# Performance work log

Measured on AMD Instinct MI355X. Metric: run time of the kernel, lower is better.

The kernel has to match this reference:

```python
import math
import jax, jax.numpy as jnp
import numpy as np

N = 100000
E_RAND = 800000
IN_F, HID, OUT_F, HEADS = 128, 64, 64, 4
NOISE_SCALE = 1.0 * math.sqrt(2.0 * math.log(1.25 / 0.05))  # dp_rate=1, eps=1, del=0.05


def setup_inputs() -> dict:
    key = jax.random.key(0)
    ks = jax.random.split(key, 12)
    x = jax.random.normal(ks[0], (N, IN_F), dtype=jnp.float32)
    src_r = jax.random.randint(ks[1], (E_RAND,), 0, N, dtype=jnp.int32)
    dst_r = jax.random.randint(ks[2], (E_RAND,), 0, N, dtype=jnp.int32)
    loops = jnp.arange(N, dtype=jnp.int32)  # add_self_loop
    src = jnp.concatenate([src_r, loops])
    dst = jnp.concatenate([dst_r, loops])
    # layer 0: GATConv(in=128, out=64, heads=4)
    s0 = 1.0 / math.sqrt(IN_F)
    W0 = jax.random.normal(ks[3], (IN_F, HEADS * HID), dtype=jnp.float32) * s0
    al0 = jax.random.normal(ks[4], (HEADS, HID), dtype=jnp.float32) * 0.1
    ar0 = jax.random.normal(ks[5], (HEADS, HID), dtype=jnp.float32) * 0.1
    b0 = jnp.zeros((HEADS * HID,), dtype=jnp.float32)
    # layer 1: GATConv(in=256, out=64, heads=1)
    s1 = 1.0 / math.sqrt(HEADS * HID)
    W1 = jax.random.normal(ks[6], (HEADS * HID, OUT_F), dtype=jnp.float32) * s1
    al1 = jax.random.normal(ks[7], (1, OUT_F), dtype=jnp.float32) * 0.1
    ar1 = jax.random.normal(ks[8], (1, OUT_F), dtype=jnp.float32) * 0.1
    b1 = jnp.zeros((OUT_F,), dtype=jnp.float32)
    # DP gaussian noise added after first GAT layer (torch.normal(0,1,x.shape))
    noise = jax.random.normal(ks[9], (N, HEADS * HID), dtype=jnp.float32)
    return {"x": x, "src": src, "dst": dst, "W0": W0, "al0": al0, "ar0": ar0,
            "b0": b0, "W1": W1, "al1": al1, "ar1": ar1, "b1": b1, "noise": noise}


def gat_conv(x, src, dst, W, al, ar, b, apply_act):
    """DGL GATConv: per-edge attention, edge softmax over dst, scatter-sum."""
    H, D = al.shape
    h = (x @ W).reshape(-1, H, D)                      # [N,H,D]
    el = jnp.sum(h * al, axis=-1)                      # [N,H]
    er = jnp.sum(h * ar, axis=-1)                      # [N,H]
    e = jax.nn.leaky_relu(el[src] + er[dst], 0.2)      # [E,H]
    emax = jax.ops.segment_max(e, dst, num_segments=N) # [N,H]
    a = jnp.exp(e - emax[dst])
    denom = jax.ops.segment_sum(a, dst, num_segments=N)
    alpha = a / denom[dst]                             # [E,H] edge softmax
    msg = h[src] * alpha[:, :, None]                   # [E,H,D]
    out = jax.ops.segment_sum(msg, dst, num_segments=N) + b.reshape(1, H, D)
    if apply_act:
        out = jax.nn.leaky_relu(out, 0.01)             # F.leaky_relu default slope
    return out.reshape(-1, H * D)                      # flatten(1)


def reference(x, src, dst, W0, al0, ar0, b0, W1, al1, ar1, b1, noise):
    h = gat_conv(x, src, dst, W0, al0, ar0, b0, apply_act=True)   # [N, 256]
    h = h + NOISE_SCALE * noise                                   # DP noise after layer 0
    out = gat_conv(h, src, dst, W1, al1, ar1, b1, apply_act=False)  # [N, 64]
    return out
```

## Files before the change

kernel.cpp:

```cpp
#include <hip/hip_runtime.h>
#include <hip/hip_bf16.h>
#include <math.h>

#define IN_F 128
#define HID 64
#define HEADS 4
#define HD0 (HEADS * HID)
#define OUT_F 64
#define NOISE_SCALE 2.5372725354060904f

typedef __bf16 bf16x8 __attribute__((ext_vector_type(8)));
typedef float f32x4 __attribute__((ext_vector_type(4)));

__device__ __forceinline__ float bf2f(unsigned short u) {
    return __uint_as_float(((unsigned)u) << 16);
}
__device__ __forceinline__ unsigned short f2bf(float f) {
    unsigned u = __float_as_uint(f);
    u = u + 0x7fffu + ((u >> 16) & 1u);
    return (unsigned short)(u >> 16);
}

__device__ __forceinline__ void acc8(float* acc, const uint4& u, float wt) {
    acc[0] += wt * __uint_as_float(u.x << 16);
    acc[1] += wt * __uint_as_float(u.x & 0xffff0000u);
    acc[2] += wt * __uint_as_float(u.y << 16);
    acc[3] += wt * __uint_as_float(u.y & 0xffff0000u);
    acc[4] += wt * __uint_as_float(u.z << 16);
    acc[5] += wt * __uint_as_float(u.z & 0xffff0000u);
    acc[6] += wt * __uint_as_float(u.w << 16);
    acc[7] += wt * __uint_as_float(u.w & 0xffff0000u);
}

__global__ __launch_bounds__(256) void cast_bf16_kernel(
    const float* __restrict__ in, unsigned short* __restrict__ out, size_t n8,
    int* __restrict__ deg, int N) {
    size_t i = (size_t)blockIdx.x * 256 + threadIdx.x;
    if (i < (size_t)N) deg[i] = 0;
    if (i >= n8) return;
    const float4 a = ((const float4*)in)[i * 2];
    const float4 b = ((const float4*)in)[i * 2 + 1];
    ushort4 o0, o1;
    o0.x = f2bf(a.x); o0.y = f2bf(a.y); o0.z = f2bf(a.z); o0.w = f2bf(a.w);
    o1.x = f2bf(b.x); o1.y = f2bf(b.y); o1.z = f2bf(b.z); o1.w = f2bf(b.w);
    ((ushort4*)out)[i * 2] = o0;
    ((ushort4*)out)[i * 2 + 1] = o1;
}

__global__ __launch_bounds__(256) void tcast2_kernel(
    const float* __restrict__ W0, unsigned short* __restrict__ W0t,
    const float* __restrict__ W1, unsigned short* __restrict__ W1t) {
    int i = blockIdx.x * 256 + threadIdx.x;
    if (i < IN_F * HD0) {
        int n = i / IN_F, k = i % IN_F;
        W0t[i] = f2bf(W0[(size_t)k * HD0 + n]);
    } else {
        int j = i - IN_F * HD0;
        if (j < HD0 * OUT_F) {
            int n = j / HD0, k = j % HD0;
            W1t[j] = f2bf(W1[(size_t)k * OUT_F + n]);
        }
    }
}

template <int K, int H>
__global__ __launch_bounds__(256) void gemm_fused_kernel(
    const unsigned short* __restrict__ A, const unsigned short* __restrict__ Bt,
    unsigned short* __restrict__ C, const float* __restrict__ al,
    const float* __restrict__ ar, float* __restrict__ el,
    float* __restrict__ er, int M, int NC) {
    constexpr int BSTR = K + 8;
    constexpr int ASTR = 40;
    __shared__ __align__(16) unsigned short Bs[64 * BSTR];
    __shared__ __align__(16) unsigned short As[128 * ASTR];
    const int tid = threadIdx.x;
    const int lane = tid & 63, w = tid >> 6;
    const int row0 = blockIdx.y * 128;
    const int n0 = blockIdx.x * 64;
    for (int i = tid; i < 64 * (K / 8); i += 256) {
        int n = i / (K / 8), kc = i % (K / 8);
        *(uint4*)(Bs + n * BSTR + kc * 8) =
            *(const uint4*)(Bt + (size_t)(n0 + n) * K + kc * 8);
    }
    f32x4 acc[2][4] = {};
    const int q = lane >> 4, c = lane & 15;
    const int r_st = tid >> 1, hh = tid & 1;
    for (int k0 = 0; k0 < K; k0 += 32) {
        int gr = row0 + r_st;
        uint4 av0 = make_uint4(0, 0, 0, 0), av1 = make_uint4(0, 0, 0, 0);
        if (gr < M) {
            const unsigned short* ap = A + (size_t)gr * K + k0 + hh * 16;
            av0 = *(const uint4*)(ap);
            av1 = *(const uint4*)(ap + 8);
        }
        __syncthreads();
        *(uint4*)(As + r_st * ASTR + hh * 16) = av0;
        *(uint4*)(As + r_st * ASTR + hh * 16 + 8) = av1;
        __syncthreads();
        bf16x8 af[2], bfr[4];
        af[0] = *(const bf16x8*)(As + (w * 32 + c) * ASTR + q * 8);
        af[1] = *(const bf16x8*)(As + (w * 32 + 16 + c) * ASTR + q * 8);
#pragma unroll
        for (int nt = 0; nt < 4; ++nt)
            bfr[nt] = *(const bf16x8*)(Bs + (nt * 16 + c) * BSTR + k0 + q * 8);
#pragma unroll
        for (int mt = 0; mt < 2; ++mt)
#pragma unroll
            for (int nt = 0; nt < 4; ++nt)
                acc[mt][nt] = __builtin_amdgcn_mfma_f32_16x16x32_bf16(
                    af[mt], bfr[nt], acc[mt][nt], 0, 0, 0);
    }
    float alv[4], arv[4];
#pragma unroll
    for (int nt = 0; nt < 4; ++nt) {
        alv[nt] = al[n0 + nt * 16 + c];
        arv[nt] = ar[n0 + nt * 16 + c];
    }
    const int head = n0 >> 6;
#pragma unroll
    for (int mt = 0; mt < 2; ++mt) {
#pragma unroll
        for (int r = 0; r < 4; ++r) {
            int grow = row0 + w * 32 + mt * 16 + q * 4 + r;
            bool ok = grow < M;
            float elp = 0.f, erp = 0.f;
#pragma unroll
            for (int nt = 0; nt < 4; ++nt) {
                float v = acc[mt][nt][r];
                elp += v * alv[nt];
                erp += v * arv[nt];
                if (ok) C[(size_t)grow * NC + n0 + nt * 16 + c] = f2bf(v);
            }
#pragma unroll
            for (int o = 8; o > 0; o >>= 1) {
                elp += __shfl_down(elp, o, 16);
                erp += __shfl_down(erp, o, 16);
            }
            if (c == 0 && ok) {
                el[(size_t)grow * H + head] = elp;
                er[(size_t)grow * H + head] = erp;
            }
        }
    }
}

__global__ __launch_bounds__(256) void degree_kernel(
    const int* __restrict__ dst, int* __restrict__ deg, int E) {
    int e = blockIdx.x * 256 + threadIdx.x;
    if (e < E) atomicAdd(&deg[dst[e]], 1);
}

__global__ __launch_bounds__(256) void scan_block_kernel(
    const int* __restrict__ deg, int* __restrict__ off,
    int* __restrict__ bsum, int N) {
    __shared__ int s[256];
    int i = blockIdx.x * 256 + threadIdx.x;
    int v = (i < N) ? deg[i] : 0;
    s[threadIdx.x] = v;
    __syncthreads();
    for (int d = 1; d < 256; d <<= 1) {
        int t = (threadIdx.x >= d) ? s[threadIdx.x - d] : 0;
        __syncthreads();
        s[threadIdx.x] += t;
        __syncthreads();
    }
    if (i < N) off[i] = s[threadIdx.x] - v;
    if (threadIdx.x == 255) bsum[blockIdx.x] = s[255];
}

__global__ __launch_bounds__(512) void scan_partials_kernel(int* __restrict__ bsum, int nb) {
    __shared__ int s[512];
    int v = (threadIdx.x < nb) ? bsum[threadIdx.x] : 0;
    s[threadIdx.x] = v;
    __syncthreads();
    for (int d = 1; d < 512; d <<= 1) {
        int t = (threadIdx.x >= d) ? s[threadIdx.x - d] : 0;
        __syncthreads();
        s[threadIdx.x] += t;
        __syncthreads();
    }
    if (threadIdx.x < nb) bsum[threadIdx.x] = s[threadIdx.x] - v;
}

__global__ __launch_bounds__(256) void add_offsets_kernel(
    int* __restrict__ off, int* __restrict__ cur,
    const int* __restrict__ bsum, int N, int E) {
    int i = blockIdx.x * 256 + threadIdx.x;
    if (i < N) {
        int v = off[i] + bsum[blockIdx.x];
        off[i] = v;
        cur[i] = v;
    }
    if (i == 0) off[N] = E;
}

__global__ __launch_bounds__(256) void fill_csr_kernel(
    const int* __restrict__ src, const int* __restrict__ dst,
    int* __restrict__ cur, int* __restrict__ csr_src, int E) {
    int e = blockIdx.x * 256 + threadIdx.x;
    if (e >= E) return;
    int d = dst[e];
    int pos = atomicAdd(&cur[d], 1);
    csr_src[pos] = src[e];
}

__global__ __launch_bounds__(256) void agg0_kernel(
    const int* __restrict__ off, const int* __restrict__ csr_src,
    const unsigned short* __restrict__ h,
    const float* __restrict__ el,
    const float* __restrict__ er,
    const float* __restrict__ b0, const float* __restrict__ noise,
    unsigned short* __restrict__ out, int N) {
    int gt = blockIdx.x * 256 + threadIdx.x;
    int n = gt >> 5;
    if (n >= N) return;
    const int lane = gt & 31;
    const int hd = lane >> 3;
    const int f0 = lane << 3;
    const float ern = er[(size_t)n * 4 + hd];
    const int beg = off[n];
    const int last = off[n + 1] - 1;
    float acc[8] = {0.f, 0.f, 0.f, 0.f, 0.f, 0.f, 0.f, 0.f};
    float l = 0.f;
    for (int p = beg; p <= last; p += 4) {
        int i1 = p + 1, i2 = p + 2, i3 = p + 3;
        const bool v1 = i1 <= last, v2 = i2 <= last, v3 = i3 <= last;
        i1 = v1 ? i1 : last;
        i2 = v2 ? i2 : last;
        i3 = v3 ? i3 : last;
        const int s0 = csr_src[p],  s1 = csr_src[i1];
        const int s2 = csr_src[i2], s3 = csr_src[i3];
        float e0 = el[(size_t)s0 * 4 + hd] + ern;
        float e1 = el[(size_t)s1 * 4 + hd] + ern;
        float e2 = el[(size_t)s2 * 4 + hd] + ern;
        float e3 = el[(size_t)s3 * 4 + hd] + ern;
        const uint4 u0 = *(const uint4*)(h + (size_t)s0 * HD0 + f0);
        const uint4 u1 = *(const uint4*)(h + (size_t)s1 * HD0 + f0);
        const uint4 u2 = *(const uint4*)(h + (size_t)s2 * HD0 + f0);
        const uint4 u3 = *(const uint4*)(h + (size_t)s3 * HD0 + f0);
        e0 = e0 > 0.f ? e0 : 0.2f * e0;
        e1 = e1 > 0.f ? e1 : 0.2f * e1;
        e2 = e2 > 0.f ? e2 : 0.2f * e2;
        e3 = e3 > 0.f ? e3 : 0.2f * e3;
        const float w0 = __expf(e0);
        const float w1 = v1 ? __expf(e1) : 0.f;
        const float w2 = v2 ? __expf(e2) : 0.f;
        const float w3 = v3 ? __expf(e3) : 0.f;
        acc8(acc, u0, w0);
        acc8(acc, u1, w1);
        acc8(acc, u2, w2);
        acc8(acc, u3, w3);
        l += (w0 + w1) + (w2 + w3);
    }
    const float rd = 1.f / l;
    const float4 ba = *(const float4*)(b0 + f0);
    const float4 bb = *(const float4*)(b0 + f0 + 4);
    const float4 na = *(const float4*)(noise + (size_t)n * HD0 + f0);
    const float4 nb = *(const float4*)(noise + (size_t)n * HD0 + f0 + 4);
    float o[8];
    o[0] = acc[0] * rd + ba.x;
    o[1] = acc[1] * rd + ba.y;
    o[2] = acc[2] * rd + ba.z;
    o[3] = acc[3] * rd + ba.w;
    o[4] = acc[4] * rd + bb.x;
    o[5] = acc[5] * rd + bb.y;
    o[6] = acc[6] * rd + bb.z;
    o[7] = acc[7] * rd + bb.w;
#pragma unroll
    for (int j = 0; j < 8; ++j) o[j] = o[j] > 0.f ? o[j] : 0.01f * o[j];
    o[0] += NOISE_SCALE * na.x;
    o[1] += NOISE_SCALE * na.y;
    o[2] += NOISE_SCALE * na.z;
    o[3] += NOISE_SCALE * na.w;
    o[4] += NOISE_SCALE * nb.x;
    o[5] += NOISE_SCALE * nb.y;
    o[6] += NOISE_SCALE * nb.z;
    o[7] += NOISE_SCALE * nb.w;
    uint4 ov;
    ov.x = (unsigned)f2bf(o[0]) | ((unsigned)f2bf(o[1]) << 16);
    ov.y = (unsigned)f2bf(o[2]) | ((unsigned)f2bf(o[3]) << 16);
    ov.z = (unsigned)f2bf(o[4]) | ((unsigned)f2bf(o[5]) << 16);
    ov.w = (unsigned)f2bf(o[6]) | ((unsigned)f2bf(o[7]) << 16);
    *(uint4*)(out + (size_t)n * HD0 + f0) = ov;
}

__global__ __launch_bounds__(256) void agg1_kernel(
    const int* __restrict__ off, const int* __restrict__ csr_src,
    const unsigned short* __restrict__ h,
    const float* __restrict__ el,
    const float* __restrict__ er,
    const float* __restrict__ b1, float* __restrict__ out, int N) {
    int gt = blockIdx.x * 256 + threadIdx.x;
    int n = gt >> 4;
    if (n >= N) return;
    const int lane = gt & 15;
    const int f0 = lane << 2;
    const float ern = er[n];
    const int beg = off[n];
    const int last = off[n + 1] - 1;
    float a0 = 0.f, a1 = 0.f, a2 = 0.f, a3 = 0.f, l = 0.f;
    for (int p = beg; p <= last; p += 4) {
        int i1 = p + 1, i2 = p + 2, i3 = p + 3;
        const bool v1 = i1 <= last, v2 = i2 <= last, v3 = i3 <= last;
        i1 = v1 ? i1 : last;
        i2 = v2 ? i2 : last;
        i3 = v3 ? i3 : last;
        const int s0 = csr_src[p],  s1 = csr_src[i1];
        const int s2 = csr_src[i2], s3 = csr_src[i3];
        float e0 = el[s0] + ern;
        float e1 = el[s1] + ern;
        float e2 = el[s2] + ern;
        float e3 = el[s3] + ern;
        const ushort4 u0 = *(const ushort4*)(h + (size_t)s0 * 64 + f0);
        const ushort4 u1 = *(const ushort4*)(h + (size_t)s1 * 64 + f0);
        const ushort4 u2 = *(const ushort4*)(h + (size_t)s2 * 64 + f0);
        const ushort4 u3 = *(const ushort4*)(h + (size_t)s3 * 64 + f0);
        e0 = e0 > 0.f ? e0 : 0.2f * e0;
        e1 = e1 > 0.f ? e1 : 0.2f * e1;
        e2 = e2 > 0.f ? e2 : 0.2f * e2;
        e3 = e3 > 0.f ? e3 : 0.2f * e3;
        const float w0 = __expf(e0);
        const float w1 = v1 ? __expf(e1) : 0.f;
        const float w2 = v2 ? __expf(e2) : 0.f;
        const float w3 = v3 ? __expf(e3) : 0.f;
        a0 += w0 * bf2f(u0.x) + w1 * bf2f(u1.x) + w2 * bf2f(u2.x) + w3 * bf2f(u3.x);
        a1 += w0 * bf2f(u0.y) + w1 * bf2f(u1.y) + w2 * bf2f(u2.y) + w3 * bf2f(u3.y);
        a2 += w0 * bf2f(u0.z) + w1 * bf2f(u1.z) + w2 * bf2f(u2.z) + w3 * bf2f(u3.z);
        a3 += w0 * bf2f(u0.w) + w1 * bf2f(u1.w) + w2 * bf2f(u2.w) + w3 * bf2f(u3.w);
        l += (w0 + w1) + (w2 + w3);
    }
    const float rd = 1.f / l;
    const float4 bv = *(const float4*)(b1 + f0);
    float4 o;
    o.x = a0 * rd + bv.x;
    o.y = a1 * rd + bv.y;
    o.z = a2 * rd + bv.z;
    o.w = a3 * rd + bv.w;
    *(float4*)(out + (size_t)n * 64 + f0) = o;
}

extern "C" void kernel_launch(void* const* d_in, const int* in_sizes, int n_in,
                              void* d_out, int out_size, void* d_ws, size_t ws_size,
                              hipStream_t stream) {
    const float* x     = (const float*)d_in[0];
    const int*   src   = (const int*)d_in[1];
    const int*   dst   = (const int*)d_in[2];
    const float* W0    = (const float*)d_in[3];
    const float* al0   = (const float*)d_in[4];
    const float* ar0   = (const float*)d_in[5];
    const float* b0    = (const float*)d_in[6];
    const float* W1    = (const float*)d_in[7];
    const float* al1   = (const float*)d_in[8];
    const float* ar1   = (const float*)d_in[9];
    const float* b1    = (const float*)d_in[10];
    const float* noise = (const float*)d_in[11];

    const int N = in_sizes[0] / IN_F;
    const int E = in_sizes[1];
    const int NB = (N + 255) / 256;

    char* p = (char*)d_ws;
    unsigned short* x_bf   = (unsigned short*)p; p += (size_t)N * IN_F * 2;
    unsigned short* h0     = (unsigned short*)p; p += (size_t)N * HD0 * 2;
    unsigned short* agg0b  = (unsigned short*)p; p += (size_t)N * HD0 * 2;
    unsigned short* h1     = (unsigned short*)p; p += (size_t)N * OUT_F * 2;
    unsigned short* W0t    = (unsigned short*)p; p += (size_t)IN_F * HD0 * 2;
    unsigned short* W1t    = (unsigned short*)p; p += (size_t)HD0 * OUT_F * 2;
    float* el     = (float*)p; p += (size_t)N * HEADS * 4;
    float* er     = (float*)p; p += (size_t)N * HEADS * 4;
    int* deg    = (int*)p; p += (size_t)N * 4;
    int* cur    = (int*)p; p += (size_t)N * 4;
    int* off    = (int*)p; p += ((size_t)N + 4) * 4;
    int* bsum   = (int*)p; p += 512 * 4;
    int* csr_src= (int*)p; p += (size_t)E * 4;

    {
        size_t n8 = (size_t)N * IN_F / 8;
        cast_bf16_kernel<<<(unsigned)((n8 + 255) / 256), 256, 0, stream>>>(
            x, x_bf, n8, deg, N);
    }
    tcast2_kernel<<<(IN_F * HD0 + HD0 * OUT_F + 255) / 256, 256, 0, stream>>>(
        W0, W0t, W1, W1t);

    degree_kernel<<<(E + 255) / 256, 256, 0, stream>>>(dst, deg, E);
    scan_block_kernel<<<NB, 256, 0, stream>>>(deg, off, bsum, N);
    scan_partials_kernel<<<1, 512, 0, stream>>>(bsum, NB);
    add_offsets_kernel<<<NB, 256, 0, stream>>>(off, cur, bsum, N, E);
    fill_csr_kernel<<<(E + 255) / 256, 256, 0, stream>>>(src, dst, cur, csr_src, E);

    const int MB = (N + 127) / 128;

    {
        dim3 grid(HD0 / 64, MB);
        gemm_fused_kernel<IN_F, HEADS><<<grid, 256, 0, stream>>>(
            x_bf, W0t, h0, al0, ar0, el, er, N, HD0);
    }
    agg0_kernel<<<(unsigned)(((size_t)N * 32 + 255) / 256), 256, 0, stream>>>(
        off, csr_src, h0, el, er, b0, noise, agg0b, N);

    {
        dim3 grid(OUT_F / 64, MB);
        gemm_fused_kernel<HD0, 1><<<grid, 256, 0, stream>>>(
            agg0b, W1t, h1, al1, ar1, el, er, N, OUT_F);
    }
    agg1_kernel<<<(unsigned)(((size_t)N * 16 + 255) / 256), 256, 0, stream>>>(
        off, csr_src, h1, el, er, b1, (float*)d_out, N);
}
```

Measured before the change: 435.2 us.

## Split edge loops across two thread groups, widen GEMM tile, merge prep kernels

Both aggregation kernels now assign two thread groups per node. Each group handles alternating chunks of four edges, and the partial sums are combined with xor shuffles before the output is written. The aim is more memory-level parallelism on the gather-bound edge loops, paid for with twice the threads and an extra reduction. The layer-0 GEMM now covers 128 output columns (two heads) per block so each A tile is reused across more MFMAs, which costs more shared memory and registers. The bf16 cast and the weight-transpose kernels are merged into one launch.

```diff
diff --git a/kernel.cpp b/kernel.cpp
--- a/kernel.cpp
+++ b/kernel.cpp
@@ -32,30 +32,29 @@
     acc[7] += wt * __uint_as_float(u.w & 0xffff0000u);
 }
 
-__global__ __launch_bounds__(256) void cast_bf16_kernel(
+__global__ __launch_bounds__(256) void prep_kernel(
     const float* __restrict__ in, unsigned short* __restrict__ out, size_t n8,
-    int* __restrict__ deg, int N) {
-    size_t i = (size_t)blockIdx.x * 256 + threadIdx.x;
-    if (i < (size_t)N) deg[i] = 0;
-    if (i >= n8) return;
-    const float4 a = ((const float4*)in)[i * 2];
-    const float4 b = ((const float4*)in)[i * 2 + 1];
-    ushort4 o0, o1;
-    o0.x = f2bf(a.x); o0.y = f2bf(a.y); o0.z = f2bf(a.z); o0.w = f2bf(a.w);
-    o1.x = f2bf(b.x); o1.y = f2bf(b.y); o1.z = f2bf(b.z); o1.w = f2bf(b.w);
-    ((ushort4*)out)[i * 2] = o0;
-    ((ushort4*)out)[i * 2 + 1] = o1;
-}
-
-__global__ __launch_bounds__(256) void tcast2_kernel(
+    int* __restrict__ deg, int N, int nb_cast,
     const float* __restrict__ W0, unsigned short* __restrict__ W0t,
     const float* __restrict__ W1, unsigned short* __restrict__ W1t) {
-    int i = blockIdx.x * 256 + threadIdx.x;
-    if (i < IN_F * HD0) {
+    const int b = blockIdx.x;
+    if (b < nb_cast) {
+        size_t i = (size_t)b * 256 + threadIdx.x;
+        if (i < (size_t)N) deg[i] = 0;
+        if (i >= n8) return;
+        const float4 a = ((const float4*)in)[i * 2];
+        const float4 c = ((const float4*)in)[i * 2 + 1];
+        ushort4 o0, o1;
+        o0.x = f2bf(a.x); o0.y = f2bf(a.y); o0.z = f2bf(a.z); o0.w = f2bf(a.w);
+        o1.x = f2bf(c.x); o1.y = f2bf(c.y); o1.z = f2bf(c.z); o1.w = f2bf(c.w);
+        ((ushort4*)out)[i * 2] = o0;
+        ((ushort4*)out)[i * 2 + 1] = o1;
+    } else if (b < nb_cast + (IN_F * HD0) / 256) {
+        int i = (b - nb_cast) * 256 + threadIdx.x;
         int n = i / IN_F, k = i % IN_F;
         W0t[i] = f2bf(W0[(size_t)k * HD0 + n]);
     } else {
-        int j = i - IN_F * HD0;
+        int j = (b - nb_cast - (IN_F * HD0) / 256) * 256 + threadIdx.x;
         if (j < HD0 * OUT_F) {
             int n = j / HD0, k = j % HD0;
             W1t[j] = f2bf(W1[(size_t)k * OUT_F + n]);
@@ -63,7 +62,7 @@
     }
 }
 
-template <int K, int H>
+template <int K, int H, int NT>
 __global__ __launch_bounds__(256) void gemm_fused_kernel(
     const unsigned short* __restrict__ A, const unsigned short* __restrict__ Bt,
     unsigned short* __restrict__ C, const float* __restrict__ al,
@@ -71,18 +70,19 @@
     float* __restrict__ er, int M, int NC) {
     constexpr int BSTR = K + 8;
     constexpr int ASTR = 40;
-    __shared__ __align__(16) unsigned short Bs[64 * BSTR];
+    constexpr int NROWS = 64 * NT;
+    __shared__ __align__(16) unsigned short Bs[NROWS * BSTR];
     __shared__ __align__(16) unsigned short As[128 * ASTR];
     const int tid = threadIdx.x;
     const int lane = tid & 63, w = tid >> 6;
     const int row0 = blockIdx.y * 128;
-    const int n0 = blockIdx.x * 64;
-    for (int i = tid; i < 64 * (K / 8); i += 256) {
+    const int n0 = blockIdx.x * NROWS;
+    for (int i = tid; i < NROWS * (K / 8); i += 256) {
         int n = i / (K / 8), kc = i % (K / 8);
         *(uint4*)(Bs + n * BSTR + kc * 8) =
             *(const uint4*)(Bt + (size_t)(n0 + n) * K + kc * 8);
     }
-    f32x4 acc[2][4] = {};
+    f32x4 acc[2][4 * NT] = {};
     const int q = lane >> 4, c = lane & 15;
     const int r_st = tid >> 1, hh = tid & 1;
     for (int k0 = 0; k0 < K; k0 += 32) {
@@ -97,48 +97,52 @@
         *(uint4*)(As + r_st * ASTR + hh * 16) = av0;
         *(uint4*)(As + r_st * ASTR + hh * 16 + 8) = av1;
         __syncthreads();
-        bf16x8 af[2], bfr[4];
+        bf16x8 af[2], bfr[4 * NT];
         af[0] = *(const bf16x8*)(As + (w * 32 + c) * ASTR + q * 8);
         af[1] = *(const bf16x8*)(As + (w * 32 + 16 + c) * ASTR + q * 8);
 #pragma unroll
-        for (int nt = 0; nt < 4; ++nt)
+        for (int nt = 0; nt < 4 * NT; ++nt)
             bfr[nt] = *(const bf16x8*)(Bs + (nt * 16 + c) * BSTR + k0 + q * 8);
 #pragma unroll
         for (int mt = 0; mt < 2; ++mt)
 #pragma unroll
-            for (int nt = 0; nt < 4; ++nt)
+            for (int nt = 0; nt < 4 * NT; ++nt)
                 acc[mt][nt] = __builtin_amdgcn_mfma_f32_16x16x32_bf16(
                     af[mt], bfr[nt], acc[mt][nt], 0, 0, 0);
     }
-    float alv[4], arv[4];
-#pragma unroll
-    for (int nt = 0; nt < 4; ++nt) {
+    float alv[4 * NT], arv[4 * NT];
+#pragma unroll
+    for (int nt = 0; nt < 4 * NT; ++nt) {
         alv[nt] = al[n0 + nt * 16 + c];
         arv[nt] = ar[n0 + nt * 16 + c];
     }
-    const int head = n0 >> 6;
+    const int headbase = n0 >> 6;
 #pragma unroll
     for (int mt = 0; mt < 2; ++mt) {
 #pragma unroll
         for (int r = 0; r < 4; ++r) {
             int grow = row0 + w * 32 + mt * 16 + q * 4 + r;
             bool ok = grow < M;
-            float elp = 0.f, erp = 0.f;
-#pragma unroll
-            for (int nt = 0; nt < 4; ++nt) {
-                float v = acc[mt][nt][r];
-                elp += v * alv[nt];
-                erp += v * arv[nt];
-                if (ok) C[(size_t)grow * NC + n0 + nt * 16 + c] = f2bf(v);
-            }
-#pragma unroll
-            for (int o = 8; o > 0; o >>= 1) {
-                elp += __shfl_down(elp, o, 16);
-                erp += __shfl_down(erp, o, 16);
-            }
-            if (c == 0 && ok) {
-                el[(size_t)grow * H + head] = elp;
-                er[(size_t)grow * H + head] = erp;
+#pragma unroll
+            for (int g = 0; g < NT; ++g) {
+                float elp = 0.f, erp = 0.f;
+#pragma unroll
+                for (int t = 0; t < 4; ++t) {
+                    int nt = g * 4 + t;
+                    float v = acc[mt][nt][r];
+                    elp += v * alv[nt];
+                    erp += v * arv[nt];
+                    if (ok) C[(size_t)grow * NC + n0 + nt * 16 + c] = f2bf(v);
+                }
+#pragma unroll
+                for (int o = 8; o > 0; o >>= 1) {
+                    elp += __shfl_down(elp, o, 16);
+                    erp += __shfl_down(erp, o, 16);
+                }
+                if (c == 0 && ok) {
+                    el[(size_t)grow * H + headbase + g] = elp;
+                    er[(size_t)grow * H + headbase + g] = erp;
+                }
             }
         }
     }
@@ -212,17 +216,19 @@
     const float* __restrict__ b0, const float* __restrict__ noise,
     unsigned short* __restrict__ out, int N) {
     int gt = blockIdx.x * 256 + threadIdx.x;
-    int n = gt >> 5;
+    int n = gt >> 6;
     if (n >= N) return;
-    const int lane = gt & 31;
-    const int hd = lane >> 3;
-    const int f0 = lane << 3;
+    const int lane = gt & 63;
+    const int grp = lane >> 5;
+    const int fl = lane & 31;
+    const int hd = fl >> 3;
+    const int f0 = fl << 3;
     const float ern = er[(size_t)n * 4 + hd];
     const int beg = off[n];
     const int last = off[n + 1] - 1;
     float acc[8] = {0.f, 0.f, 0.f, 0.f, 0.f, 0.f, 0.f, 0.f};
     float l = 0.f;
-    for (int p = beg; p <= last; p += 4) {
+    for (int p = beg + grp * 4; p <= last; p += 8) {
         int i1 = p + 1, i2 = p + 2, i3 = p + 3;
         const bool v1 = i1 <= last, v2 = i2 <= last, v3 = i3 <= last;
         i1 = v1 ? i1 : last;
@@ -252,6 +258,10 @@
         acc8(acc, u3, w3);
         l += (w0 + w1) + (w2 + w3);
     }
+    l += __shfl_xor(l, 32);
+#pragma unroll
+    for (int j = 0; j < 8; ++j) acc[j] += __shfl_xor(acc[j], 32);
+    if (grp != 0) return;
     const float rd = 1.f / l;
     const float4 ba = *(const float4*)(b0 + f0);
     const float4 bb = *(const float4*)(b0 + f0 + 4);
@@ -291,15 +301,17 @@
     const float* __restrict__ er,
     const float* __restrict__ b1, float* __restrict__ out, int N) {
     int gt = blockIdx.x * 256 + threadIdx.x;
-    int n = gt >> 4;
+    int n = gt >> 5;
     if (n >= N) return;
-    const int lane = gt & 15;
-    const int f0 = lane << 2;
+    const int lane5 = gt & 31;
+    const int grp = lane5 >> 4;
+    const int fl = lane5 & 15;
+    const int f0 = fl << 2;
     const float ern = er[n];
     const int beg = off[n];
     const int last = off[n + 1] - 1;
     float a0 = 0.f, a1 = 0.f, a2 = 0.f, a3 = 0.f, l = 0.f;
-    for (int p = beg; p <= last; p += 4) {
+    for (int p = beg + grp * 4; p <= last; p += 8) {
         int i1 = p + 1, i2 = p + 2, i3 = p + 3;
         const bool v1 = i1 <= last, v2 = i2 <= last, v3 = i3 <= last;
         i1 = v1 ? i1 : last;
@@ -329,6 +341,12 @@
         a3 += w0 * bf2f(u0.w) + w1 * bf2f(u1.w) + w2 * bf2f(u2.w) + w3 * bf2f(u3.w);
         l += (w0 + w1) + (w2 + w3);
     }
+    l += __shfl_xor(l, 16);
+    a0 += __shfl_xor(a0, 16);
+    a1 += __shfl_xor(a1, 16);
+    a2 += __shfl_xor(a2, 16);
+    a3 += __shfl_xor(a3, 16);
+    if (grp != 0) return;
     const float rd = 1.f / l;
     const float4 bv = *(const float4*)(b1 + f0);
     float4 o;
@@ -376,11 +394,12 @@
 
     {
         size_t n8 = (size_t)N * IN_F / 8;
-        cast_bf16_kernel<<<(unsigned)((n8 + 255) / 256), 256, 0, stream>>>(
-            x, x_bf, n8, deg, N);
-    }
-    tcast2_kernel<<<(IN_F * HD0 + HD0 * OUT_F + 255) / 256, 256, 0, stream>>>(
-        W0, W0t, W1, W1t);
+        int nb_cast = (int)((n8 + 255) / 256);
+        int nb_w0 = (IN_F * HD0) / 256;
+        int nb_w1 = (HD0 * OUT_F + 255) / 256;
+        prep_kernel<<<nb_cast + nb_w0 + nb_w1, 256, 0, stream>>>(
+            x, x_bf, n8, deg, N, nb_cast, W0, W0t, W1, W1t);
+    }
 
     degree_kernel<<<(E + 255) / 256, 256, 0, stream>>>(dst, deg, E);
     scan_block_kernel<<<NB, 256, 0, stream>>>(deg, off, bsum, N);
@@ -391,18 +410,18 @@
     const int MB = (N + 127) / 128;
 
     {
-        dim3 grid(HD0 / 64, MB);
-        gemm_fused_kernel<IN_F, HEADS><<<grid, 256, 0, stream>>>(
+        dim3 grid(HD0 / 128, MB);
+        gemm_fused_kernel<IN_F, HEADS, 2><<<grid, 256, 0, stream>>>(
             x_bf, W0t, h0, al0, ar0, el, er, N, HD0);
     }
-    agg0_kernel<<<(unsigned)(((size_t)N * 32 + 255) / 256), 256, 0, stream>>>(
+    agg0_kernel<<<(unsigned)(((size_t)N * 64 + 255) / 256), 256, 0, stream>>>(
         off, csr_src, h0, el, er, b0, noise, agg0b, N);
 
     {
         dim3 grid(OUT_F / 64, MB);
-        gemm_fused_kernel<HD0, 1><<<grid, 256, 0, stream>>>(
+        gemm_fused_kernel<HD0, 1, 1><<<grid, 256, 0, stream>>>(
             agg0b, W1t, h1, al1, ar1, el, er, N, OUT_F);
     }
-    agg1_kernel<<<(unsigned)(((size_t)N * 16 + 255) / 256), 256, 0, stream>>>(
+    agg1_kernel<<<(unsigned)(((size_t)N * 32 + 255) / 256), 256, 0, stream>>>(
         off, csr_src, h1, el, er, b1, (float*)d_out, N);
 }
```

Result: slower. 446.5 us (+2.6%).

## Fuse input bf16 cast into GEMM, widen column tile, stage output through LDS

Applied to the files above, without the earlier changes.

The layer-0 GEMM now reads the fp32 node features directly and converts them to bf16 while loading its tile. This removes the separate cast kernel and its intermediate bf16 buffer round trip. Each block now covers 128 output columns instead of 64, which halves how often each A row is re-read. Output tiles are staged in LDS so global stores become full 16-byte rows. The degree zeroing and weight transposes are merged into one prep kernel, and the noise load is marked nontemporal. The trade-off is more LDS and registers per block, plus extra synchronisation in the epilogue.

```diff
diff --git a/kernel.cpp b/kernel.cpp
--- a/kernel.cpp
+++ b/kernel.cpp
@@ -11,6 +11,8 @@
 
 typedef __bf16 bf16x8 __attribute__((ext_vector_type(8)));
 typedef float f32x4 __attribute__((ext_vector_type(4)));
+typedef float f4 __attribute__((ext_vector_type(4)));
+typedef unsigned int u4 __attribute__((ext_vector_type(4)));
 
 __device__ __forceinline__ float bf2f(unsigned short u) {
     return __uint_as_float(((unsigned)u) << 16);
@@ -32,115 +34,140 @@
     acc[7] += wt * __uint_as_float(u.w & 0xffff0000u);
 }
 
-__global__ __launch_bounds__(256) void cast_bf16_kernel(
-    const float* __restrict__ in, unsigned short* __restrict__ out, size_t n8,
-    int* __restrict__ deg, int N) {
-    size_t i = (size_t)blockIdx.x * 256 + threadIdx.x;
-    if (i < (size_t)N) deg[i] = 0;
-    if (i >= n8) return;
-    const float4 a = ((const float4*)in)[i * 2];
-    const float4 b = ((const float4*)in)[i * 2 + 1];
-    ushort4 o0, o1;
-    o0.x = f2bf(a.x); o0.y = f2bf(a.y); o0.z = f2bf(a.z); o0.w = f2bf(a.w);
-    o1.x = f2bf(b.x); o1.y = f2bf(b.y); o1.z = f2bf(b.z); o1.w = f2bf(b.w);
-    ((ushort4*)out)[i * 2] = o0;
-    ((ushort4*)out)[i * 2 + 1] = o1;
-}
-
-__global__ __launch_bounds__(256) void tcast2_kernel(
+__device__ __forceinline__ uint4 pack8(const float4& a, const float4& b) {
+    uint4 r;
+    r.x = (unsigned)f2bf(a.x) | ((unsigned)f2bf(a.y) << 16);
+    r.y = (unsigned)f2bf(a.z) | ((unsigned)f2bf(a.w) << 16);
+    r.z = (unsigned)f2bf(b.x) | ((unsigned)f2bf(b.y) << 16);
+    r.w = (unsigned)f2bf(b.z) | ((unsigned)f2bf(b.w) << 16);
+    return r;
+}
+
+__global__ __launch_bounds__(256) void prep_kernel(
+    int* __restrict__ deg, int N,
     const float* __restrict__ W0, unsigned short* __restrict__ W0t,
     const float* __restrict__ W1, unsigned short* __restrict__ W1t) {
-    int i = blockIdx.x * 256 + threadIdx.x;
-    if (i < IN_F * HD0) {
+    const int b = blockIdx.x;
+    int i = b * 256 + threadIdx.x;
+    if (i < N) deg[i] = 0;
+    if (b < (IN_F * HD0) / 256) {
         int n = i / IN_F, k = i % IN_F;
         W0t[i] = f2bf(W0[(size_t)k * HD0 + n]);
-    } else {
+    } else if (b < (IN_F * HD0) / 256 + (HD0 * OUT_F) / 256) {
         int j = i - IN_F * HD0;
-        if (j < HD0 * OUT_F) {
-            int n = j / HD0, k = j % HD0;
-            W1t[j] = f2bf(W1[(size_t)k * OUT_F + n]);
-        }
-    }
-}
-
-template <int K, int H>
+        int n = j / HD0, k = j % HD0;
+        W1t[j] = f2bf(W1[(size_t)k * OUT_F + n]);
+    }
+}
+
+template <int K, int H, int NT, bool CVT>
 __global__ __launch_bounds__(256) void gemm_fused_kernel(
-    const unsigned short* __restrict__ A, const unsigned short* __restrict__ Bt,
+    const void* __restrict__ Asrc, const unsigned short* __restrict__ Bt,
     unsigned short* __restrict__ C, const float* __restrict__ al,
     const float* __restrict__ ar, float* __restrict__ el,
     float* __restrict__ er, int M, int NC) {
     constexpr int BSTR = K + 8;
     constexpr int ASTR = 40;
-    __shared__ __align__(16) unsigned short Bs[64 * BSTR];
+    constexpr int NROWS = 64 * NT;
+    constexpr int CSTR = NROWS + 8;
+    __shared__ __align__(16) unsigned short Bs[NROWS * BSTR];
     __shared__ __align__(16) unsigned short As[128 * ASTR];
+    const unsigned short* Ab = (const unsigned short*)Asrc;
+    const float* Af = (const float*)Asrc;
     const int tid = threadIdx.x;
     const int lane = tid & 63, w = tid >> 6;
     const int row0 = blockIdx.y * 128;
-    const int n0 = blockIdx.x * 64;
-    for (int i = tid; i < 64 * (K / 8); i += 256) {
+    const int n0 = blockIdx.x * NROWS;
+    for (int i = tid; i < NROWS * (K / 8); i += 256) {
         int n = i / (K / 8), kc = i % (K / 8);
         *(uint4*)(Bs + n * BSTR + kc * 8) =
             *(const uint4*)(Bt + (size_t)(n0 + n) * K + kc * 8);
     }
-    f32x4 acc[2][4] = {};
+    f32x4 acc[2][4 * NT] = {};
     const int q = lane >> 4, c = lane & 15;
     const int r_st = tid >> 1, hh = tid & 1;
     for (int k0 = 0; k0 < K; k0 += 32) {
         int gr = row0 + r_st;
         uint4 av0 = make_uint4(0, 0, 0, 0), av1 = make_uint4(0, 0, 0, 0);
         if (gr < M) {
-            const unsigned short* ap = A + (size_t)gr * K + k0 + hh * 16;
-            av0 = *(const uint4*)(ap);
-            av1 = *(const uint4*)(ap + 8);
+            if (CVT) {
+                const float* xp = Af + (size_t)gr * K + k0 + hh * 16;
+                const float4 fa = *(const float4*)xp;
+                const float4 fb = *(const float4*)(xp + 4);
+                const float4 fc = *(const float4*)(xp + 8);
+                const float4 fd = *(const float4*)(xp + 12);
+                av0 = pack8(fa, fb);
+                av1 = pack8(fc, fd);
+            } else {
+                const unsigned short* ap = Ab + (size_t)gr * K + k0 + hh * 16;
+                av0 = *(const uint4*)(ap);
+                av1 = *(const uint4*)(ap + 8);
+            }
         }
         __syncthreads();
         *(uint4*)(As + r_st * ASTR + hh * 16) = av0;
         *(uint4*)(As + r_st * ASTR + hh * 16 + 8) = av1;
         __syncthreads();
-        bf16x8 af[2], bfr[4];
+        bf16x8 af[2], bfr[4 * NT];
         af[0] = *(const bf16x8*)(As + (w * 32 + c) * ASTR + q * 8);
         af[1] = *(const bf16x8*)(As + (w * 32 + 16 + c) * ASTR + q * 8);
 #pragma unroll
-        for (int nt = 0; nt < 4; ++nt)
+        for (int nt = 0; nt < 4 * NT; ++nt)
             bfr[nt] = *(const bf16x8*)(Bs + (nt * 16 + c) * BSTR + k0 + q * 8);
 #pragma unroll
         for (int mt = 0; mt < 2; ++mt)
 #pragma unroll
-            for (int nt = 0; nt < 4; ++nt)
+            for (int nt = 0; nt < 4 * NT; ++nt)
                 acc[mt][nt] = __builtin_amdgcn_mfma_f32_16x16x32_bf16(
                     af[mt], bfr[nt], acc[mt][nt], 0, 0, 0);
     }
-    float alv[4], arv[4];
-#pragma unroll
-    for (int nt = 0; nt < 4; ++nt) {
+    float alv[4 * NT], arv[4 * NT];
+#pragma unroll
+    for (int nt = 0; nt < 4 * NT; ++nt) {
         alv[nt] = al[n0 + nt * 16 + c];
         arv[nt] = ar[n0 + nt * 16 + c];
     }
-    const int head = n0 >> 6;
+    __syncthreads();
+    unsigned short* Cs = Bs;
+    const int headbase = n0 >> 6;
 #pragma unroll
     for (int mt = 0; mt < 2; ++mt) {
 #pragma unroll
         for (int r = 0; r < 4; ++r) {
-            int grow = row0 + w * 32 + mt * 16 + q * 4 + r;
-            bool ok = grow < M;
-            float elp = 0.f, erp = 0.f;
-#pragma unroll
-            for (int nt = 0; nt < 4; ++nt) {
-                float v = acc[mt][nt][r];
-                elp += v * alv[nt];
-                erp += v * arv[nt];
-                if (ok) C[(size_t)grow * NC + n0 + nt * 16 + c] = f2bf(v);
-            }
-#pragma unroll
-            for (int o = 8; o > 0; o >>= 1) {
-                elp += __shfl_down(elp, o, 16);
-                erp += __shfl_down(erp, o, 16);
-            }
-            if (c == 0 && ok) {
-                el[(size_t)grow * H + head] = elp;
-                er[(size_t)grow * H + head] = erp;
+            const int row = w * 32 + mt * 16 + q * 4 + r;
+            const int grow = row0 + row;
+            const bool ok = grow < M;
+#pragma unroll
+            for (int g = 0; g < NT; ++g) {
+                float elp = 0.f, erp = 0.f;
+#pragma unroll
+                for (int t = 0; t < 4; ++t) {
+                    int nt = g * 4 + t;
+                    float v = acc[mt][nt][r];
+                    elp += v * alv[nt];
+                    erp += v * arv[nt];
+                    Cs[row * CSTR + nt * 16 + c] = f2bf(v);
+                }
+#pragma unroll
+                for (int o = 8; o > 0; o >>= 1) {
+                    elp += __shfl_down(elp, o, 16);
+                    erp += __shfl_down(erp, o, 16);
+                }
+                if (c == 0 && ok) {
+                    el[(size_t)grow * H + headbase + g] = elp;
+                    er[(size_t)grow * H + headbase + g] = erp;
+                }
             }
         }
+    }
+    __syncthreads();
+    constexpr int CPR = NROWS / 8;
+    for (int i = tid; i < 128 * CPR; i += 256) {
+        int row = i / CPR, ch = i % CPR;
+        int grow = row0 + row;
+        if (grow < M)
+            *(uint4*)(C + (size_t)grow * NC + n0 + ch * 8) =
+                *(const uint4*)(Cs + row * CSTR + ch * 8);
     }
 }
 
@@ -255,8 +282,8 @@
     const float rd = 1.f / l;
     const float4 ba = *(const float4*)(b0 + f0);
     const float4 bb = *(const float4*)(b0 + f0 + 4);
-    const float4 na = *(const float4*)(noise + (size_t)n * HD0 + f0);
-    const float4 nb = *(const float4*)(noise + (size_t)n * HD0 + f0 + 4);
+    const f4 na = __builtin_nontemporal_load((const f4*)(noise + (size_t)n * HD0 + f0));
+    const f4 nb = __builtin_nontemporal_load((const f4*)(noise + (size_t)n * HD0 + f0 + 4));
     float o[8];
     o[0] = acc[0] * rd + ba.x;
     o[1] = acc[1] * rd + ba.y;
@@ -360,7 +387,6 @@
     const int NB = (N + 255) / 256;
 
     char* p = (char*)d_ws;
-    unsigned short* x_bf   = (unsigned short*)p; p += (size_t)N * IN_F * 2;
     unsigned short* h0     = (unsigned short*)p; p += (size_t)N * HD0 * 2;
     unsigned short* agg0b  = (unsigned short*)p; p += (size_t)N * HD0 * 2;
     unsigned short* h1     = (unsigned short*)p; p += (size_t)N * OUT_F * 2;
@@ -374,13 +400,7 @@
     int* bsum   = (int*)p; p += 512 * 4;
     int* csr_src= (int*)p; p += (size_t)E * 4;
 
-    {
-        size_t n8 = (size_t)N * IN_F / 8;
-        cast_bf16_kernel<<<(unsigned)((n8 + 255) / 256), 256, 0, stream>>>(
-            x, x_bf, n8, deg, N);
-    }
-    tcast2_kernel<<<(IN_F * HD0 + HD0 * OUT_F + 255) / 256, 256, 0, stream>>>(
-        W0, W0t, W1, W1t);
+    prep_kernel<<<NB, 256, 0, stream>>>(deg, N, W0, W0t, W1, W1t);
 
     degree_kernel<<<(E + 255) / 256, 256, 0, stream>>>(dst, deg, E);
     scan_block_kernel<<<NB, 256, 0, stream>>>(deg, off, bsum, N);
@@ -391,17 +411,17 @@
     const int MB = (N + 127) / 128;
 
     {
-        dim3 grid(HD0 / 64, MB);
-        gemm_fused_kernel<IN_F, HEADS><<<grid, 256, 0, stream>>>(
-            x_bf, W0t, h0, al0, ar0, el, er, N, HD0);
+        dim3 grid(HD0 / 128, MB);
+        gemm_fused_kernel<IN_F, HEADS, 2, true><<<grid, 256, 0, stream>>>(
+            (const void*)x, W0t, h0, al0, ar0, el, er, N, HD0);
     }
     agg0_kernel<<<(unsigned)(((size_t)N * 32 + 255) / 256), 256, 0, stream>>>(
         off, csr_src, h0, el, er, b0, noise, agg0b, N);
 
     {
         dim3 grid(OUT_F / 64, MB);
-        gemm_fused_kernel<HD0, 1><<<grid, 256, 0, stream>>>(
-            agg0b, W1t, h1, al1, ar1, el, er, N, OUT_F);
+        gemm_fused_kernel<HD0, 1, 1, false><<<grid, 256, 0, stream>>>(
+            (const void*)agg0b, W1t, h1, al1, ar1, el, er, N, OUT_F);
     }
     agg1_kernel<<<(unsigned)(((size_t)N * 16 + 255) / 256), 256, 0, stream>>>(
         off, csr_src, h1, el, er, b1, (float*)d_out, N);
```

Measured after the change: 431.4 us, median of 2. No clear change (-0.9%).
